# Optimization experiments

Hardware: AMD Instinct MI355X
Metric: run time of the kernel (lower is better)

## Reference

```python
import jax, jax.numpy as jnp
import numpy as np
import math

EPS = 1e-08


def setup_inputs() -> dict:
    key = jax.random.key(0)
    ks = jax.random.split(key, 5)
    N, n, d = 8, 32768, 128
    K, h, d_hat = 64, 128, 128
    return {
        "X": jax.random.normal(ks[0], (N, n, d), dtype=jnp.float32),
        "S": jax.random.normal(ks[1], (N, K, h), dtype=jnp.float32),
        "Wk": jax.random.normal(ks[2], (d, d_hat), dtype=jnp.float32) * (1.0 / math.sqrt(d)),
        "Wq": jax.random.normal(ks[3], (h, d_hat), dtype=jnp.float32) * (1.0 / math.sqrt(h)),
        "Wv": jax.random.normal(ks[4], (d, d_hat), dtype=jnp.float32) * (1.0 / math.sqrt(d)),
    }


def reference(X, S, Wk, Wq, Wv):
    # X: [N, n, d], S: [N, K, h]
    d_hat = Wk.shape[1]
    scale = 1.0 / math.sqrt(d_hat)
    k = jnp.einsum('bnd,de->bne', X, Wk)   # [N, n, d_hat]
    v = jnp.einsum('bnd,de->bne', X, Wv)   # [N, n, d_hat]
    q = jnp.einsum('bkh,he->bke', S, Wq)   # [N, K, d_hat]
    M = scale * jnp.einsum('bne,bke->bnk', k, q)  # [N, n, K]
    attn = jax.nn.sigmoid(M) + EPS
    W = attn / jnp.sum(attn, axis=2, keepdims=True)  # normalize over slots K
    S_hat = jnp.einsum('bnk,bne->bke', W, v)  # [N, K, d_hat]
    return S_hat
```

## Files before the change

### kernel.cpp

```cpp
#include <hip/hip_runtime.h>
#include <hip/hip_bf16.h>

typedef __attribute__((ext_vector_type(8))) short short8;
typedef __attribute__((ext_vector_type(4))) float f32x4;

#define N_BATCH 8
#define N_ROWS 32768
#define DDIM 128
#define KSLOT 64
#define EH 128
#define TPB 8
#define BLK_PER_B 64
#define SCALE 0.08838834764831845f

__device__ inline unsigned short f2bf(float f){
  unsigned int u = __builtin_bit_cast(unsigned int, f);
  u = (u + 0x7FFFu + ((u >> 16) & 1u)) >> 16;
  return (unsigned short)u;
}

__device__ inline unsigned int pk2bf(float lo, float hi){
  __hip_bfloat162 h = __float22bfloat162_rn(float2{lo, hi});
  unsigned int u;
  __builtin_memcpy(&u, &h, 4);
  return u;
}

__device__ inline void lds_barrier(){
  asm volatile("s_waitcnt lgkmcnt(0)" ::: "memory");
  __builtin_amdgcn_s_barrier();
}

__global__ void prep_qk_kernel(const float* __restrict__ S, const float* __restrict__ Wq,
                               const float* __restrict__ Wk, unsigned short* __restrict__ qk){
  int bs = blockIdx.x;
  __shared__ float srow[128];
  __shared__ float qrow[128];
  int t = threadIdx.x;
  srow[t] = S[bs * 128 + t];
  __syncthreads();
  float acc = 0.f;
  #pragma unroll 8
  for(int h = 0; h < 128; ++h) acc += srow[h] * Wq[h * 128 + t];
  qrow[t] = acc;
  __syncthreads();
  float acc2 = 0.f;
  #pragma unroll 8
  for(int e = 0; e < 128; ++e) acc2 += qrow[e] * Wk[t * 128 + e];
  qk[bs * 128 + t] = f2bf(acc2 * SCALE);
}

__global__ __launch_bounds__(256, 2) void sse_main_kernel(
    const float* __restrict__ X, const unsigned short* __restrict__ qkg,
    float* __restrict__ partials)
{
  __shared__ unsigned short qs[64][136];
  __shared__ unsigned short Xs[64][136];
  __shared__ unsigned short Xt[128][70];
  __shared__ unsigned short WTs[64][72];

  const int tid  = threadIdx.x;
  const int wave = tid >> 6;
  const int lane = tid & 63;
  const int l15  = lane & 15;
  const int g    = lane >> 4;
  const int l31  = lane & 31;
  const int half = lane >> 5;

  const int b  = blockIdx.x / BLK_PER_B;
  const int tb = blockIdx.x % BLK_PER_B;

  const float* Xb = X + (size_t)b * N_ROWS * DDIM;
  const unsigned short* qkb = qkg + b * KSLOT * EH;

  #pragma unroll
  for(int i = 0; i < 4; ++i){
    int o = (i * 256 + tid) * 8;
    *reinterpret_cast<short8*>(&qs[o >> 7][o & 127]) =
        *reinterpret_cast<const short8*>(qkb + o);
  }

  f32x4 sacc[8];
  #pragma unroll
  for(int i = 0; i < 8; ++i) sacc[i] = {0.f, 0.f, 0.f, 0.f};

  const float* xw = Xb + (size_t)(tb * TPB * 64 + wave * 16) * DDIM + lane * 4;

  f32x4 xa[8];
  #pragma unroll
  for(int c = 0; c < 8; ++c)
    xa[c] = *reinterpret_cast<const f32x4*>(xw + c * 256);

  lds_barrier();

  const int wr0 = wave * 16;

  #pragma unroll
  for(int tt = 0; tt < TPB; ++tt){

    #pragma unroll
    for(int c = 0; c < 8; ++c){
      const int n = wr0 + 2 * c + half;
      unsigned int u0 = pk2bf(xa[c][0], xa[c][1]);
      unsigned int u1 = pk2bf(xa[c][2], xa[c][3]);
      ushort4 p;
      __builtin_memcpy(&p, &u0, 4);
      __builtin_memcpy(reinterpret_cast<char*>(&p) + 4, &u1, 4);
      *reinterpret_cast<ushort4*>(&Xs[n][4 * l31]) = p;
      Xt[4 * l31 + 0][n] = p.x;
      Xt[4 * l31 + 1][n] = p.y;
      Xt[4 * l31 + 2][n] = p.z;
      Xt[4 * l31 + 3][n] = p.w;
    }

    if(tt + 1 < TPB){
      const float* xp = xw + (size_t)(tt + 1) * 64 * DDIM;
      #pragma unroll
      for(int c = 0; c < 8; ++c)
        xa[c] = *reinterpret_cast<const f32x4*>(xp + c * 256);
    }

    f32x4 macc[4];
    #pragma unroll
    for(int i = 0; i < 4; ++i) macc[i] = {0.f,0.f,0.f,0.f};
    #pragma unroll
    for(int step = 0; step < 4; ++step){
      short8 a = *reinterpret_cast<const short8*>(&Xs[wr0 + l15][step * 32 + g * 8]);
      #pragma unroll
      for(int st = 0; st < 4; ++st){
        short8 bq = *reinterpret_cast<const short8*>(&qs[st * 16 + l15][step * 32 + g * 8]);
        macc[st] = __builtin_amdgcn_mfma_f32_16x16x32_bf16(a, bq, macc[st], 0, 0, 0);
      }
    }

    float att[4][4];
    float rinv[4];
    #pragma unroll
    for(int st = 0; st < 4; ++st){
      #pragma unroll
      for(int r = 0; r < 4; ++r)
        att[st][r] = __builtin_amdgcn_rcpf(1.f + __expf(-macc[st][r])) + 1e-8f;
    }
    #pragma unroll
    for(int r = 0; r < 4; ++r){
      float s = att[0][r] + att[1][r] + att[2][r] + att[3][r];
      s += __shfl_xor(s, 1); s += __shfl_xor(s, 2);
      s += __shfl_xor(s, 4); s += __shfl_xor(s, 8);
      rinv[r] = __builtin_amdgcn_rcpf(s);
    }
    #pragma unroll
    for(int st = 0; st < 4; ++st){
      unsigned int u0 = pk2bf(att[st][0] * rinv[0], att[st][1] * rinv[1]);
      unsigned int u1 = pk2bf(att[st][2] * rinv[2], att[st][3] * rinv[3]);
      ushort4 wp;
      __builtin_memcpy(&wp, &u0, 4);
      __builtin_memcpy(reinterpret_cast<char*>(&wp) + 4, &u1, 4);
      *reinterpret_cast<ushort4*>(&WTs[st * 16 + l15][wave * 16 + g * 4]) = wp;
    }
    lds_barrier();

    #pragma unroll
    for(int ns = 0; ns < 2; ++ns){
      short8 af = *reinterpret_cast<const short8*>(&WTs[wr0 + l15][ns * 32 + g * 8]);
      #pragma unroll
      for(int et = 0; et < 8; ++et){
        short8 bf = *reinterpret_cast<const short8*>(&Xt[et * 16 + l15][ns * 32 + g * 8]);
        sacc[et] = __builtin_amdgcn_mfma_f32_16x16x32_bf16(af, bf, sacc[et], 0, 0, 0);
      }
    }
    lds_barrier();
  }

  float* po = partials + (size_t)blockIdx.x * (KSLOT * EH);
  #pragma unroll
  for(int et = 0; et < 8; ++et){
    #pragma unroll
    for(int r = 0; r < 4; ++r)
      po[(wave * 16 + g * 4 + r) * EH + et * 16 + l15] = sacc[et][r];
  }
}

__global__ void reduce_kernel(const float* __restrict__ partials,
                              const float* __restrict__ Wv, float* __restrict__ out){
  int bs = blockIdx.x;
  int b  = bs >> 6;
  int s  = bs & 63;
  __shared__ float Tl[128];
  int t = threadIdx.x;
  const float* pb = partials + (size_t)b * BLK_PER_B * (KSLOT * EH) + s * EH + t;
  float acc = 0.f;
  #pragma unroll 8
  for(int i = 0; i < BLK_PER_B; ++i)
    acc += pb[(size_t)i * (KSLOT * EH)];
  Tl[t] = acc;
  __syncthreads();
  float o = 0.f;
  #pragma unroll 8
  for(int d = 0; d < 128; ++d) o += Tl[d] * Wv[d * 128 + t];
  out[bs * 128 + t] = o;
}

extern "C" void kernel_launch(void* const* d_in, const int* in_sizes, int n_in,
                              void* d_out, int out_size, void* d_ws, size_t ws_size,
                              hipStream_t stream){
  const float* X  = (const float*)d_in[0];
  const float* S  = (const float*)d_in[1];
  const float* Wk = (const float*)d_in[2];
  const float* Wq = (const float*)d_in[3];
  const float* Wv = (const float*)d_in[4];
  float* out = (float*)d_out;

  char* ws = (char*)d_ws;
  unsigned short* qk = (unsigned short*)(ws);
  float* partials    = (float*)(ws + 131072);

  hipLaunchKernelGGL(prep_qk_kernel, dim3(512), dim3(128), 0, stream, S, Wq, Wk, qk);
  hipLaunchKernelGGL(sse_main_kernel, dim3(N_BATCH * BLK_PER_B), dim3(256), 0, stream,
                     X, qk, partials);
  hipLaunchKernelGGL(reduce_kernel, dim3(512), dim3(128), 0, stream, partials, Wv, out);
}
```

Baseline: 55.88 us.

## Prelayout qk as MFMA fragments read from global; double block count

The prep kernel now writes the scaled qk matrix pre-swizzled into MFMA B-operand fragment order, so the main kernel loads B fragments straight from global/L2 instead of staging qs in LDS. This removes the qs shared array and its initial barrier, cutting LDS use and possibly raising occupancy. Tiles per block drop from 8 to 4 and blocks per batch rise from 64 to 128, giving more parallelism. The cost is twice as many partials for the reduce kernel to sum, repeated global loads of qk fragments inside the inner loop, and an Xs padding change.

```diff
diff --git a/kernel.cpp b/kernel.cpp
--- a/kernel.cpp
+++ b/kernel.cpp
@@ -9,8 +9,8 @@
 #define DDIM 128
 #define KSLOT 64
 #define EH 128
-#define TPB 8
-#define BLK_PER_B 64
+#define TPB 4
+#define BLK_PER_B 128
 #define SCALE 0.08838834764831845f
 
 __device__ inline unsigned short f2bf(float f){
@@ -32,10 +32,11 @@
 }
 
 __global__ void prep_qk_kernel(const float* __restrict__ S, const float* __restrict__ Wq,
-                               const float* __restrict__ Wk, unsigned short* __restrict__ qk){
+                               const float* __restrict__ Wk, unsigned short* __restrict__ qf){
   int bs = blockIdx.x;
   __shared__ float srow[128];
   __shared__ float qrow[128];
+  __shared__ float krow[128];
   int t = threadIdx.x;
   srow[t] = S[bs * 128 + t];
   __syncthreads();
@@ -47,15 +48,25 @@
   float acc2 = 0.f;
   #pragma unroll 8
   for(int e = 0; e < 128; ++e) acc2 += qrow[e] * Wk[t * 128 + e];
-  qk[bs * 128 + t] = f2bf(acc2 * SCALE);
+  krow[t] = acc2 * SCALE;
+  __syncthreads();
+  if(t < 16){
+    int step = t >> 2, g = t & 3;
+    int b = bs >> 6, s = bs & 63;
+    int st = s >> 4, l15 = s & 15;
+    short8 v;
+    #pragma unroll
+    for(int e = 0; e < 8; ++e) v[e] = (short)f2bf(krow[step * 32 + g * 8 + e]);
+    *reinterpret_cast<short8*>(qf + (size_t)b * 8192 +
+        (size_t)(((st * 4 + step) * 64 + g * 16 + l15) * 8)) = v;
+  }
 }
 
 __global__ __launch_bounds__(256, 2) void sse_main_kernel(
-    const float* __restrict__ X, const unsigned short* __restrict__ qkg,
+    const float* __restrict__ X, const unsigned short* __restrict__ qf,
     float* __restrict__ partials)
 {
-  __shared__ unsigned short qs[64][136];
-  __shared__ unsigned short Xs[64][136];
+  __shared__ unsigned short Xs[64][138];
   __shared__ unsigned short Xt[128][70];
   __shared__ unsigned short WTs[64][72];
 
@@ -71,14 +82,7 @@
   const int tb = blockIdx.x % BLK_PER_B;
 
   const float* Xb = X + (size_t)b * N_ROWS * DDIM;
-  const unsigned short* qkb = qkg + b * KSLOT * EH;
-
-  #pragma unroll
-  for(int i = 0; i < 4; ++i){
-    int o = (i * 256 + tid) * 8;
-    *reinterpret_cast<short8*>(&qs[o >> 7][o & 127]) =
-        *reinterpret_cast<const short8*>(qkb + o);
-  }
+  const unsigned short* qkb = qf + (size_t)b * 8192;
 
   f32x4 sacc[8];
   #pragma unroll
@@ -90,8 +94,6 @@
   #pragma unroll
   for(int c = 0; c < 8; ++c)
     xa[c] = *reinterpret_cast<const f32x4*>(xw + c * 256);
-
-  lds_barrier();
 
   const int wr0 = wave * 16;
 
@@ -128,7 +130,8 @@
       short8 a = *reinterpret_cast<const short8*>(&Xs[wr0 + l15][step * 32 + g * 8]);
       #pragma unroll
       for(int st = 0; st < 4; ++st){
-        short8 bq = *reinterpret_cast<const short8*>(&qs[st * 16 + l15][step * 32 + g * 8]);
+        short8 bq = *reinterpret_cast<const short8*>(qkb +
+            (size_t)(((st * 4 + step) * 64 + lane) * 8));
         macc[st] = __builtin_amdgcn_mfma_f32_16x16x32_bf16(a, bq, macc[st], 0, 0, 0);
       }
     }
@@ -211,11 +214,11 @@
   float* out = (float*)d_out;
 
   char* ws = (char*)d_ws;
-  unsigned short* qk = (unsigned short*)(ws);
+  unsigned short* qf = (unsigned short*)(ws);
   float* partials    = (float*)(ws + 131072);
 
-  hipLaunchKernelGGL(prep_qk_kernel, dim3(512), dim3(128), 0, stream, S, Wq, Wk, qk);
+  hipLaunchKernelGGL(prep_qk_kernel, dim3(512), dim3(128), 0, stream, S, Wq, Wk, qf);
   hipLaunchKernelGGL(sse_main_kernel, dim3(N_BATCH * BLK_PER_B), dim3(256), 0, stream,
-                     X, qk, partials);
+                     X, qf, partials);
   hipLaunchKernelGGL(reduce_kernel, dim3(512), dim3(128), 0, stream, partials, Wv, out);
 }
```

After: 75.69 us. 1.35x slower.
